# Optimization experiments

Measured on AMD Instinct MI355X. Metric: run time of the kernel, lower is better.

Reference implementation:

```python
import jax, jax.numpy as jnp
import numpy as np

# FP4 E2M1 constants (from the torch module)
EXP_BITS = 2
EXP_BIAS = 1          # 2**(EXP_BITS-1) - 1
MANT_BITS = 1
MAX_EXP_FIELD = 3     # (1 << EXP_BITS) - 1
MIN_NORMAL_EXP = 0    # 1 - EXP_BIAS
FP4_MAX = 6.0         # (1 + 1/2) * 2**(MAX_EXP_FIELD-1 - EXP_BIAS + 1) = 1.5 * 4
GROUP = 128


def fp4_quant_dequant(x):
    """Faithful composition of _float_to_fp4 followed by _fp4_to_float (E2M1,
    subnormal-aware), expressed in float arithmetic (bit pack/unpack cancels)."""
    a = jnp.abs(x)
    zero_mask = a == 0
    a_safe = jnp.where(zero_mask, jnp.float32(1e-8), a)
    e = jnp.floor(jnp.log2(a_safe))                      # unbiased exponent
    is_sub = e < MIN_NORMAL_EXP
    e_c = jnp.clip(e, MIN_NORMAL_EXP, MAX_EXP_FIELD - EXP_BIAS)
    mant_scale = float(1 << MANT_BITS)                   # 2.0
    mant_normal = jnp.clip(jnp.round((a_safe / jnp.exp2(e_c) - 1.0) * mant_scale), 0.0, mant_scale - 1.0)
    mant_sub = jnp.clip(jnp.round(a_safe / (2.0 ** MIN_NORMAL_EXP) * mant_scale), 0.0, mant_scale - 1.0)
    mant = jnp.where(is_sub, mant_sub, mant_normal)
    # decode (_fp4_to_float): normals (1 + m/2)*2^(e), subnormals (m/2)*2^(1-bias)
    val_normal = (1.0 + mant / mant_scale) * jnp.exp2(e_c)
    val_sub = (mant / mant_scale) * (2.0 ** (1 - EXP_BIAS))
    val = jnp.where(is_sub, val_sub, val_normal)
    val = jnp.where(x < 0, -val, val)
    return jnp.where(zero_mask, jnp.zeros_like(val), val)


def setup_inputs() -> dict:
    key = jax.random.key(0)
    k1, k2, k3 = jax.random.split(key, 3)
    x = jax.random.normal(k1, (4096, 4096), dtype=jnp.float32)
    weight = jax.random.normal(k2, (4096, 4096), dtype=jnp.float32) * 0.02
    b = jax.random.normal(k3, (4096,), dtype=jnp.float32)
    return {"x": x, "weight": weight, "b": b}


def reference(x, weight, b):
    out_f, in_f = weight.shape
    wg = weight.reshape(out_f, in_f // GROUP, GROUP)
    amax = jnp.max(jnp.abs(wg), axis=-1, keepdims=True)       # [out, groups, 1]
    scale = jnp.where(amax == 0, jnp.float32(1.0), amax / FP4_MAX)
    w_deq = (fp4_quant_dequant(wg / scale) * scale).reshape(out_f, in_f)
    return x @ w_deq.T + b
```

## Files before the change

### kernel.cpp

```cpp
#include <hip/hip_runtime.h>
#include <hip/hip_bf16.h>
#include <stdint.h>

#define KDIM 4096
#define NDIM 4096
#define MDIM 4096
#define BM 256
#define BN 256
#define BK 64

typedef __attribute__((ext_vector_type(8))) short bf16x8;
typedef __attribute__((ext_vector_type(4))) float f32x4;


__device__ __forceinline__ unsigned short bf16bits(float f) {
    union { float f; uint32_t u; } c; c.f = f;
    uint32_t u = c.u;
    uint32_t r = (u + 0x7fffu + ((u >> 16) & 1u)) >> 16;
    return (unsigned short)r;
}

__device__ __forceinline__ float fp4qd(float x) {
    float a = fabsf(x);
    if (a == 0.0f) return 0.0f;
    float e = floorf(log2f(a));
    float val;
    if (e < 0.0f) {
        float mant = fminf(fmaxf(rintf(a * 2.0f), 0.0f), 1.0f);
        val = mant * 0.5f;
    } else {
        float ec = fminf(e, 2.0f);
        float p  = exp2f(ec);
        float mant = fminf(fmaxf(rintf((a / p - 1.0f) * 2.0f), 0.0f), 1.0f);
        val = (1.0f + 0.5f * mant) * p;
    }
    return (x < 0.0f) ? -val : val;
}

__device__ __forceinline__ void gld16(void* lds, const void* g) {
    __builtin_amdgcn_global_load_lds(
        (const __attribute__((address_space(1))) unsigned int*)g,
        (__attribute__((address_space(3))) unsigned int*)lds,
        16, 0, 0);
}

__global__ __launch_bounds__(256) void wdeq_kernel(const float* __restrict__ W,
                                                   unsigned short* __restrict__ Wq) {
    int grp = blockIdx.x * 4 + (threadIdx.x >> 6);
    int l = threadIdx.x & 63;
    const float* gp = W + (size_t)grp * 128 + l * 2;
    float2 v = *(const float2*)gp;
    float am = fmaxf(fabsf(v.x), fabsf(v.y));
    #pragma unroll
    for (int s = 32; s; s >>= 1) am = fmaxf(am, __shfl_xor(am, s));
    float scale = (am == 0.0f) ? 1.0f : am / 6.0f;
    float q0 = fp4qd(v.x / scale) * scale;
    float q1 = fp4qd(v.y / scale) * scale;
    ushort2 o;
    o.x = bf16bits(q0);
    o.y = bf16bits(q1);
    *(ushort2*)(Wq + (size_t)grp * 128 + l * 2) = o;
}

__global__ __launch_bounds__(256) void xcvt_kernel(const float* __restrict__ X,
                                                   unsigned short* __restrict__ Xb) {
    size_t i = (size_t)(blockIdx.x * 256 + threadIdx.x) * 4;
    float4 v = *(const float4*)(X + i);
    ushort4 o;
    o.x = bf16bits(v.x); o.y = bf16bits(v.y);
    o.z = bf16bits(v.z); o.w = bf16bits(v.w);
    *(ushort4*)(Xb + i) = o;
}


#define BAR()   __builtin_amdgcn_s_barrier()
#define LGKM0() asm volatile("s_waitcnt lgkmcnt(0)" ::: "memory")
#define VM4()   asm volatile("s_waitcnt vmcnt(4)" ::: "memory")
#define SCH0()  __builtin_amdgcn_sched_barrier(0)
#define PRIO(x) __builtin_amdgcn_s_setprio(x)

__global__ __launch_bounds__(512, 2) void gemm256(const unsigned short* __restrict__ A,
                                                  const unsigned short* __restrict__ B,
                                                  const float* __restrict__ bias,
                                                  float* __restrict__ C) {
    __shared__ __attribute__((aligned(16))) char smem[2][2][2][16384];
    char* sm = (char*)&smem[0][0][0][0];

    const int t = threadIdx.x;
    const int l = t & 63;
    const int w = __builtin_amdgcn_readfirstlane(t >> 6);
    const int wm = w >> 2;
    const int wn = w & 3;

    int bid = blockIdx.x;
    int swz = (bid & 7) * 32 + (bid >> 3);
    int brow = (swz >> 4) * BM;
    int bcol = (swz & 15) * BN;

    const int lr8  = l >> 3;
    const int slot = l & 7;
    const int scol = (slot ^ lr8) << 3;
    const unsigned short* pA = A + (size_t)(brow + w * 8 + lr8) * KDIM + scol;
    const unsigned short* pB = B + (size_t)(bcol + w * 8 + lr8) * KDIM + scol;

#define STAGE(b, op, h, kt) do {                                               \
    const unsigned short* _s = ((op) ? pB : pA)                                \
        + (size_t)(h) * 128 * KDIM + (size_t)(kt) * BK;                        \
    gld16(sm + (b) * 65536 + (op) * 32768 + (h) * 16384 + w * 1024, _s);       \
    gld16(sm + (b) * 65536 + (op) * 32768 + (h) * 16384 + 8192 + w * 1024,     \
          _s + (size_t)64 * KDIM);                                             \
} while (0)

    const int fr  = l & 15;
    const int fq  = l >> 4;
    const int kx0 = ((fq    ) ^ (fr & 7)) << 4;
    const int kx1 = ((fq + 4) ^ (fr & 7)) << 4;
    const int frA = fr * 128;

#define RD_A(b, mh) do {                                                        \
    const char* _p = sm + (b) * 65536 + wm * 16384 + (mh) * 8192 + frA;         \
    _Pragma("unroll")                                                           \
    for (int m = 0; m < 4; ++m) {                                               \
        a[m][0] = *(const bf16x8*)(_p + m * 2048 + kx0);                        \
        a[m][1] = *(const bf16x8*)(_p + m * 2048 + kx1);                        \
    }                                                                           \
} while (0)

#define RD_B(b, nh, arr) do {                                                   \
    const char* _p = sm + (b) * 65536 + 32768 + (wn >> 1) * 16384               \
                     + (wn & 1) * 8192 + (nh) * 4096 + frA;                     \
    _Pragma("unroll")                                                           \
    for (int n = 0; n < 2; ++n) {                                               \
        arr[n][0] = *(const bf16x8*)(_p + n * 2048 + kx0);                      \
        arr[n][1] = *(const bf16x8*)(_p + n * 2048 + kx1);                      \
    }                                                                           \
} while (0)

#define MM(mh, nh, arr)                                                         \
    _Pragma("unroll")                                                           \
    for (int m = 0; m < 4; ++m)                                                 \
        _Pragma("unroll")                                                       \
        for (int n = 0; n < 2; ++n)                                             \
            _Pragma("unroll")                                                   \
            for (int ks = 0; ks < 2; ++ks)                                      \
                acc[(mh) * 4 + m][(nh) * 2 + n] =                               \
                    __builtin_amdgcn_mfma_f32_16x16x32_bf16(                    \
                        a[m][ks], arr[n][ks], acc[(mh) * 4 + m][(nh) * 2 + n],  \
                        0, 0, 0);

    f32x4 acc[8][4];
    #pragma unroll
    for (int m = 0; m < 8; ++m)
        #pragma unroll
        for (int n = 0; n < 4; ++n)
            acc[m][n] = f32x4{0.f, 0.f, 0.f, 0.f};

    bf16x8 a[4][2], bA[2][2], bB[2][2];

    STAGE(0, 0, 0, 0); STAGE(0, 0, 1, 0); STAGE(0, 1, 0, 0); STAGE(0, 1, 1, 0);
    STAGE(1, 1, 0, 1); STAGE(1, 0, 0, 1);
    VM4();
    BAR(); SCH0();

    for (int it = 0; it < 32; ++it) {
        const int k1 = 2 * it + 1;
        const int k2 = (2 * it + 2) & 63;
        const int k3 = (2 * it + 3) & 63;

        RD_A(0, 0); RD_B(0, 0, bA); STAGE(1, 0, 1, k1);
        BAR(); LGKM0(); SCH0(); PRIO(1); MM(0, 0, bA); PRIO(0); BAR(); SCH0();
        RD_B(0, 1, bB); STAGE(1, 1, 1, k1);
        BAR(); LGKM0(); SCH0(); PRIO(1); MM(0, 1, bB); PRIO(0); BAR(); SCH0();
        RD_A(0, 1); STAGE(0, 1, 0, k2);
        BAR(); LGKM0(); SCH0(); PRIO(1); MM(1, 1, bB); PRIO(0); BAR(); SCH0();
        STAGE(0, 0, 0, k2);
        BAR(); SCH0(); PRIO(1); MM(1, 0, bA); PRIO(0); VM4(); BAR(); SCH0();

        RD_A(1, 0); RD_B(1, 0, bA); STAGE(0, 0, 1, k2);
        BAR(); LGKM0(); SCH0(); PRIO(1); MM(0, 0, bA); PRIO(0); BAR(); SCH0();
        RD_B(1, 1, bB); STAGE(0, 1, 1, k2);
        BAR(); LGKM0(); SCH0(); PRIO(1); MM(0, 1, bB); PRIO(0); BAR(); SCH0();
        RD_A(1, 1); STAGE(1, 1, 0, k3);
        BAR(); LGKM0(); SCH0(); PRIO(1); MM(1, 1, bB); PRIO(0); BAR(); SCH0();
        STAGE(1, 0, 0, k3);
        BAR(); SCH0(); PRIO(1); MM(1, 0, bA); PRIO(0); VM4(); BAR(); SCH0();
    }

    float bb[4];
    #pragma unroll
    for (int n = 0; n < 4; ++n) bb[n] = bias[bcol + wn * 64 + n * 16 + fr];
    #pragma unroll
    for (int mi = 0; mi < 8; ++mi) {
        #pragma unroll
        for (int q = 0; q < 4; ++q) {
            int row = brow + wm * 128 + mi * 16 + fq * 4 + q;
            float* crow = C + (size_t)row * NDIM + bcol + wn * 64;
            #pragma unroll
            for (int n = 0; n < 4; ++n)
                crow[n * 16 + fr] = acc[mi][n][q] + bb[n];
        }
    }
}

extern "C" void kernel_launch(void* const* d_in, const int* in_sizes, int n_in,
                              void* d_out, int out_size, void* d_ws, size_t ws_size,
                              hipStream_t stream) {
    const float* x = (const float*)d_in[0];
    const float* w = (const float*)d_in[1];
    const float* b = (const float*)d_in[2];
    float* out = (float*)d_out;

    unsigned short* xb = (unsigned short*)d_ws;
    unsigned short* wq = xb + (size_t)NDIM * KDIM;

    xcvt_kernel<<<MDIM * KDIM / 4 / 256, 256, 0, stream>>>(x, xb);
    wdeq_kernel<<<NDIM * (KDIM / 128) / 4, 256, 0, stream>>>(w, wq);
    gemm256<<<(MDIM / BM) * (NDIM / BN), 512, 0, stream>>>(xb, wq, b, out);
}
```

Baseline: 157.8 us.

## Restage GEMM LDS loads in 64-row slabs with reordered prefetch schedule

Splits each 128-row staging unit into 64-row slabs and changes the shared-memory layout to match. It reorders which slabs are prefetched in each phase of the 8-phase main loop, relaxes the global-load wait from vmcnt(4) to vmcnt(6), and adds a partial lgkmcnt(8) wait. Some sched_barrier fences are also removed. The goal is finer-grained overlap between global-to-LDS copies and MFMA work, at the risk of new LDS read/write hazards in the changed buffer reuse order.

```diff
diff --git a/kernel.cpp b/kernel.cpp
--- a/kernel.cpp
+++ b/kernel.cpp
@@ -73,17 +73,18 @@
 }
 
 
-#define BAR()   __builtin_amdgcn_s_barrier()
-#define LGKM0() asm volatile("s_waitcnt lgkmcnt(0)" ::: "memory")
-#define VM4()   asm volatile("s_waitcnt vmcnt(4)" ::: "memory")
-#define SCH0()  __builtin_amdgcn_sched_barrier(0)
-#define PRIO(x) __builtin_amdgcn_s_setprio(x)
+#define BAR()    __builtin_amdgcn_s_barrier()
+#define LGKM0()  asm volatile("s_waitcnt lgkmcnt(0)" ::: "memory")
+#define LGKM8()  asm volatile("s_waitcnt lgkmcnt(8)" ::: "memory")
+#define VM6()    asm volatile("s_waitcnt vmcnt(6)" ::: "memory")
+#define SCH0()   __builtin_amdgcn_sched_barrier(0)
+#define PRIO(x)  __builtin_amdgcn_s_setprio(x)
 
 __global__ __launch_bounds__(512, 2) void gemm256(const unsigned short* __restrict__ A,
                                                   const unsigned short* __restrict__ B,
                                                   const float* __restrict__ bias,
                                                   float* __restrict__ C) {
-    __shared__ __attribute__((aligned(16))) char smem[2][2][2][16384];
+    __shared__ __attribute__((aligned(16))) char smem[2][2][4][8192];
     char* sm = (char*)&smem[0][0][0][0];
 
     const int t = threadIdx.x;
@@ -103,12 +104,10 @@
     const unsigned short* pA = A + (size_t)(brow + w * 8 + lr8) * KDIM + scol;
     const unsigned short* pB = B + (size_t)(bcol + w * 8 + lr8) * KDIM + scol;
 
-#define STAGE(b, op, h, kt) do {                                               \
+#define STAGE64(b, op, slab, kt) do {                                          \
     const unsigned short* _s = ((op) ? pB : pA)                                \
-        + (size_t)(h) * 128 * KDIM + (size_t)(kt) * BK;                        \
-    gld16(sm + (b) * 65536 + (op) * 32768 + (h) * 16384 + w * 1024, _s);       \
-    gld16(sm + (b) * 65536 + (op) * 32768 + (h) * 16384 + 8192 + w * 1024,     \
-          _s + (size_t)64 * KDIM);                                             \
+        + (size_t)((slab) * 64) * KDIM + (size_t)(kt) * BK;                    \
+    gld16(sm + (b) * 65536 + (op) * 32768 + (slab) * 8192 + w * 1024, _s);     \
 } while (0)
 
     const int fr  = l & 15;
@@ -127,8 +126,7 @@
 } while (0)
 
 #define RD_B(b, nh, arr) do {                                                   \
-    const char* _p = sm + (b) * 65536 + 32768 + (wn >> 1) * 16384               \
-                     + (wn & 1) * 8192 + (nh) * 4096 + frA;                     \
+    const char* _p = sm + (b) * 65536 + 32768 + wn * 8192 + (nh) * 4096 + frA;  \
     _Pragma("unroll")                                                           \
     for (int n = 0; n < 2; ++n) {                                               \
         arr[n][0] = *(const bf16x8*)(_p + n * 2048 + kx0);                      \
@@ -157,33 +155,60 @@
 
     bf16x8 a[4][2], bA[2][2], bB[2][2];
 
-    STAGE(0, 0, 0, 0); STAGE(0, 0, 1, 0); STAGE(0, 1, 0, 0); STAGE(0, 1, 1, 0);
-    STAGE(1, 1, 0, 1); STAGE(1, 0, 0, 1);
-    VM4();
-    BAR(); SCH0();
+    STAGE64(0, 0, 0, 0); STAGE64(0, 0, 2, 0); STAGE64(0, 1, 0, 0); STAGE64(0, 1, 1, 0);
+    STAGE64(0, 1, 2, 0); STAGE64(0, 1, 3, 0); STAGE64(0, 0, 1, 0); STAGE64(0, 0, 3, 0);
+    STAGE64(1, 0, 0, 1); STAGE64(1, 0, 2, 1); STAGE64(1, 1, 0, 1); STAGE64(1, 1, 1, 1);
+    STAGE64(1, 1, 2, 1); STAGE64(1, 1, 3, 1);
+    VM6();
+    BAR();
 
     for (int it = 0; it < 32; ++it) {
         const int k1 = 2 * it + 1;
         const int k2 = (2 * it + 2) & 63;
         const int k3 = (2 * it + 3) & 63;
 
-        RD_A(0, 0); RD_B(0, 0, bA); STAGE(1, 0, 1, k1);
-        BAR(); LGKM0(); SCH0(); PRIO(1); MM(0, 0, bA); PRIO(0); BAR(); SCH0();
-        RD_B(0, 1, bB); STAGE(1, 1, 1, k1);
-        BAR(); LGKM0(); SCH0(); PRIO(1); MM(0, 1, bB); PRIO(0); BAR(); SCH0();
-        RD_A(0, 1); STAGE(0, 1, 0, k2);
-        BAR(); LGKM0(); SCH0(); PRIO(1); MM(1, 1, bB); PRIO(0); BAR(); SCH0();
-        STAGE(0, 0, 0, k2);
-        BAR(); SCH0(); PRIO(1); MM(1, 0, bA); PRIO(0); VM4(); BAR(); SCH0();
-
-        RD_A(1, 0); RD_B(1, 0, bA); STAGE(0, 0, 1, k2);
-        BAR(); LGKM0(); SCH0(); PRIO(1); MM(0, 0, bA); PRIO(0); BAR(); SCH0();
-        RD_B(1, 1, bB); STAGE(0, 1, 1, k2);
-        BAR(); LGKM0(); SCH0(); PRIO(1); MM(0, 1, bB); PRIO(0); BAR(); SCH0();
-        RD_A(1, 1); STAGE(1, 1, 0, k3);
-        BAR(); LGKM0(); SCH0(); PRIO(1); MM(1, 1, bB); PRIO(0); BAR(); SCH0();
-        STAGE(1, 0, 0, k3);
-        BAR(); SCH0(); PRIO(1); MM(1, 0, bA); PRIO(0); VM4(); BAR(); SCH0();
+        RD_A(0, 0); RD_B(0, 0, bA);
+        STAGE64(1, 0, 1, k1); STAGE64(1, 0, 3, k1);
+        LGKM8();
+        BAR(); LGKM0(); SCH0();
+        PRIO(1); MM(0, 0, bA); PRIO(0);
+        BAR();
+        RD_B(0, 1, bB);
+        STAGE64(0, 0, 0, k2); STAGE64(0, 0, 2, k2);
+        BAR(); LGKM0(); SCH0();
+        PRIO(1); MM(0, 1, bB); PRIO(0);
+        BAR();
+        RD_A(0, 1);
+        STAGE64(0, 1, 0, k2); STAGE64(0, 1, 1, k2);
+        BAR(); LGKM0(); SCH0();
+        PRIO(1); MM(1, 1, bB); PRIO(0);
+        BAR();
+        STAGE64(0, 1, 2, k2); STAGE64(0, 1, 3, k2);
+        BAR(); SCH0();
+        PRIO(1); MM(1, 0, bA); PRIO(0);
+        VM6();
+        BAR();
+        RD_A(1, 0); RD_B(1, 0, bA);
+        STAGE64(0, 0, 1, k2); STAGE64(0, 0, 3, k2);
+        LGKM8();
+        BAR(); LGKM0(); SCH0();
+        PRIO(1); MM(0, 0, bA); PRIO(0);
+        BAR();
+        RD_B(1, 1, bB);
+        STAGE64(1, 0, 0, k3); STAGE64(1, 0, 2, k3);
+        BAR(); LGKM0(); SCH0();
+        PRIO(1); MM(0, 1, bB); PRIO(0);
+        BAR();
+        RD_A(1, 1);
+        STAGE64(1, 1, 0, k3); STAGE64(1, 1, 1, k3);
+        BAR(); LGKM0(); SCH0();
+        PRIO(1); MM(1, 1, bB); PRIO(0);
+        BAR();
+        STAGE64(1, 1, 2, k3); STAGE64(1, 1, 3, k3);
+        BAR(); SCH0();
+        PRIO(1); MM(1, 0, bA); PRIO(0);
+        VM6();
+        BAR();
     }
 
     float bb[4];
```

Result: no change. 157.5 us (-0.2%).
